# Optimization experiments

Hardware: AMD Instinct MI355X
Metric: run time of the kernel (lower is better)

The kernel has to match this reference:

```python
import jax, jax.numpy as jnp
import numpy as np

NUM_HEADS = 12
HEAD_DIM = 64
HIDDEN = NUM_HEADS * HEAD_DIM
AGENT_NUM = 40
MAX_POS = 2048
SCALE = HEAD_DIM ** -0.5


def _split_heads(x):
    # [b, s, hidden] -> [b, h, s, d]
    b, s, _ = x.shape
    return x.reshape(b, s, NUM_HEADS, HEAD_DIM).transpose(0, 2, 1, 3)


def _agent_pool(q, agent_num):
    # F.interpolate(q[None], size=(agent_num, dim), mode='bilinear', align_corners=False)
    # width (dim) is unchanged so it reduces to 1D linear interp along seq axis.
    b, s, dim = q.shape
    src = (jnp.arange(agent_num, dtype=q.dtype) + 0.5) * (s / agent_num) - 0.5
    src = jnp.clip(src, 0.0, s - 1.0)
    lo = jnp.floor(src).astype(jnp.int32)
    hi = jnp.minimum(lo + 1, s - 1)
    w = (src - lo.astype(q.dtype))[None, :, None]  # [1, A, 1]
    return q[:, lo, :] * (1.0 - w) + q[:, hi, :] * w  # [b, A, dim]


def setup_inputs() -> dict:
    key = jax.random.key(0)
    ks = jax.random.split(key, 6)
    bs, S = 16, 2048
    return {
        "hidden_states": jax.random.normal(ks[0], (bs, S, HIDDEN), jnp.float32),
        "attention_mask": jnp.zeros((bs, 1, 1, S), jnp.float32),
        "Wq": jax.random.normal(ks[1], (HIDDEN, HIDDEN), jnp.float32) * 0.02,
        "bq": jnp.zeros((HIDDEN,), jnp.float32),
        "Wk": jax.random.normal(ks[2], (HIDDEN, HIDDEN), jnp.float32) * 0.02,
        "bk": jnp.zeros((HIDDEN,), jnp.float32),
        "Wv": jax.random.normal(ks[3], (HIDDEN, HIDDEN), jnp.float32) * 0.02,
        "bv": jnp.zeros((HIDDEN,), jnp.float32),
        "dist_emb": jax.random.normal(ks[4], (2 * MAX_POS - 1, HEAD_DIM), jnp.float32) * 0.02,
    }


def reference(hidden_states, attention_mask, Wq, bq, Wk, bk, Wv, bv, dist_emb):
    bs, S, dim = hidden_states.shape
    q = hidden_states @ Wq + bq          # [b, S, hidden] (== query_layer flattened back)
    k = hidden_states @ Wk + bk
    v = hidden_states @ Wv + bv
    q_layer = _split_heads(q)            # [b, h, S, d]
    k_layer = _split_heads(k)
    v_layer = _split_heads(v)

    agent = _agent_pool(q, AGENT_NUM)    # [b, A, hidden]
    agent_layer = _split_heads(agent)    # [b, h, A, d]

    # stage 1: agent -> KV, with relative-key position bias
    d1 = jnp.arange(AGENT_NUM)[:, None] - jnp.arange(S)[None, :] + (MAX_POS - 1)
    pe1 = dist_emb[d1]                   # [A, S, d]
    bias1 = jnp.einsum('bhad,asd->bhas', agent_layer, pe1)
    score1 = jnp.einsum('bhad,bhsd->bhas', agent_layer * SCALE, k_layer) + bias1
    score1 = score1 + attention_mask     # [b,1,1,S] broadcasts over (h, A)
    p1 = jax.nn.softmax(score1, axis=-1)
    agent_v = jnp.einsum('bhas,bhsd->bhad', p1, v_layer)  # [b, h, A, d]

    # stage 2: query -> agents, with relative-key position bias
    d2 = jnp.arange(S)[:, None] - jnp.arange(AGENT_NUM)[None, :] + (MAX_POS - 1)
    pe2 = dist_emb[d2]                   # [S, A, d]
    bias2 = jnp.einsum('bhsd,sad->bhsa', q_layer, pe2)
    score2 = jnp.einsum('bhsd,bhad->bhsa', q_layer * SCALE, agent_layer) + bias2
    q_mask = jnp.swapaxes(attention_mask, -1, -2)  # [b,1,S,1]
    score2 = score2 + q_mask
    p2 = jax.nn.softmax(score2, axis=-1)
    x = jnp.einsum('bhsa,bhad->bhsd', p2, agent_v)  # [b, h, S, d]
    return x.transpose(0, 2, 1, 3).reshape(bs, S, dim)
```

## Files before the change

kernel.cpp:

```cpp
#include <hip/hip_runtime.h>
#include <math.h>

#define B_ 16
#define S_ 2048
#define H_ 12
#define D_ 64
#define HID 768
#define A_ 40
#define SCALE_ 0.125f
#define CH1 8
#define SUBT 64
#define NSUB 4

typedef __attribute__((ext_vector_type(8))) short short8v;
typedef __attribute__((ext_vector_type(4))) float f32x4;
typedef __attribute__((ext_vector_type(16))) float f32x16;

__device__ __forceinline__ unsigned f2bf_bits(float x) {
    unsigned u = __float_as_uint(x);
    return (u + 0x7FFFu + ((u >> 16) & 1u)) >> 16;
}

__device__ __forceinline__ void split1(float v, unsigned short& h, unsigned short& l) {
    __bf16 bh = (__bf16)v;
    float hf = (float)bh;
    __bf16 bl = (__bf16)(v - hf);
    h = __builtin_bit_cast(unsigned short, bh);
    l = __builtin_bit_cast(unsigned short, bl);
}

__device__ __forceinline__ void split8c(const float* x, int4& hi, int4& lo) {
    unsigned h[8], l[8];
#pragma unroll
    for (int i = 0; i < 8; i++) {
        __bf16 bh = (__bf16)x[i];
        float hf = (float)bh;
        __bf16 bl = (__bf16)(x[i] - hf);
        h[i] = (unsigned)__builtin_bit_cast(unsigned short, bh);
        l[i] = (unsigned)__builtin_bit_cast(unsigned short, bl);
    }
    hi = make_int4((int)(h[0] | (h[1] << 16)), (int)(h[2] | (h[3] << 16)),
                   (int)(h[4] | (h[5] << 16)), (int)(h[6] | (h[7] << 16)));
    lo = make_int4((int)(l[0] | (l[1] << 16)), (int)(l[2] | (l[3] << 16)),
                   (int)(l[4] | (l[5] << 16)), (int)(l[6] | (l[7] << 16)));
}

__global__ void wt_convert(const float* __restrict__ Wq, const float* __restrict__ Wk,
                           const float* __restrict__ Wv,
                           unsigned short* __restrict__ Wth, unsigned short* __restrict__ Wtl)
{
    int idx = blockIdx.x * 256 + threadIdx.x;
    if (idx >= 3 * 192 * 768) return;
    int n  = idx % 768;
    int kc = (idx / 768) % 192;
    int z  = idx / (768 * 192);
    const float* W = (z == 0) ? Wq : (z == 1) ? Wk : Wv;
    unsigned short h4[4], l4[4];
#pragma unroll
    for (int i = 0; i < 4; i++) {
        float x = W[(size_t)(4 * kc + i) * HID + n];
        unsigned hb = f2bf_bits(x);
        float hf = __uint_as_float(hb << 16);
        h4[i] = (unsigned short)hb;
        l4[i] = (unsigned short)f2bf_bits(x - hf);
    }
    size_t o = ((size_t)z * HID + n) * HID + 4 * kc;
    *(ushort4*)&Wth[o] = make_ushort4(h4[0], h4[1], h4[2], h4[3]);
    *(ushort4*)&Wtl[o] = make_ushort4(l4[0], l4[1], l4[2], l4[3]);
}

__global__ void dist_frag(const float* __restrict__ dist,
                          unsigned short* __restrict__ DFh, unsigned short* __restrict__ DFl)
{
    int g = blockIdx.x * 256 + threadIdx.x;
    if (g >= 256 * 2 * 64) return;
    int lane = g & 63;
    int ks = (g >> 6) & 1;
    int u  = g >> 7;
    int row = 8 + u * 16 + (lane & 15);
    int col = ks * 32 + ((lane >> 4) << 3);
    float xv[8];
#pragma unroll
    for (int j = 0; j < 8; j++)
        xv[j] = (row < 4095) ? dist[(size_t)row * D_ + col + j] : 0.f;
    int4 hi, lo;
    split8c(xv, hi, lo);
    *(int4*)&DFh[(size_t)g * 8] = hi;
    *(int4*)&DFl[(size_t)g * 8] = lo;
}

__global__ void dist_frag0(const float* __restrict__ dist,
                           unsigned short* __restrict__ Dh, unsigned short* __restrict__ Dl)
{
    int g = blockIdx.x * 256 + threadIdx.x;
    if (g >= 131 * 2 * 64) return;
    int lane = g & 63;
    int ks = (g >> 6) & 1;
    int u  = g >> 7;
    int row = u * 16 + (lane & 15);
    int col = ks * 32 + ((lane >> 4) << 3);
    float xv[8];
#pragma unroll
    for (int j = 0; j < 8; j++) xv[j] = dist[(size_t)row * D_ + col + j];
    int4 hi, lo;
    split8c(xv, hi, lo);
    *(int4*)&Dh[(size_t)g * 8] = hi;
    *(int4*)&Dl[(size_t)g * 8] = lo;
}

__global__ void ag_frag(const float* __restrict__ Ag,
                        unsigned short* __restrict__ Gh, unsigned short* __restrict__ Gl,
                        float scale)
{
    int g = blockIdx.x * 256 + threadIdx.x;
    if (g >= 192 * 3 * 2 * 64) return;
    int lane = g & 63;
    int r = g >> 6;
    int ks = r & 1; r >>= 1;
    int at = r % 3;
    int bh = r / 3;
    int a = at * 16 + (lane & 15);
    int col = ks * 32 + ((lane >> 4) << 3);
    float xv[8];
#pragma unroll
    for (int j = 0; j < 8; j++)
        xv[j] = (a < A_) ? scale * Ag[((size_t)bh * A_ + a) * D_ + col + j] : 0.f;
    int4 hi, lo;
    split8c(xv, hi, lo);
    *(int4*)&Gh[(size_t)g * 8] = hi;
    *(int4*)&Gl[(size_t)g * 8] = lo;
}

__global__ void avt_frag(const float* __restrict__ AgV,
                         unsigned short* __restrict__ Vh, unsigned short* __restrict__ Vl)
{
    int g = blockIdx.x * 256 + threadIdx.x;
    if (g >= 192 * 4 * 2 * 64) return;
    int lane = g & 63;
    int r = g >> 6;
    int ks = r & 1; r >>= 1;
    int nt = r & 3;
    int bh = r >> 2;
    int d = nt * 16 + (lane & 15);
    int a0 = ks * 32 + ((lane >> 4) << 3);
    float xv[8];
#pragma unroll
    for (int j = 0; j < 8; j++) {
        int a = a0 + j;
        xv[j] = (a < A_) ? AgV[((size_t)bh * A_ + a) * D_ + d] : 0.f;
    }
    int4 hi, lo;
    split8c(xv, hi, lo);
    *(int4*)&Vh[(size_t)g * 8] = hi;
    *(int4*)&Vl[(size_t)g * 8] = lo;
}

__global__ __launch_bounds__(512, 2) void qkv_z(
    const float* __restrict__ X,
    const unsigned short* __restrict__ Wth, const unsigned short* __restrict__ Wtl,
    const float* __restrict__ bq, const float* __restrict__ bk, const float* __restrict__ bv,
    float* __restrict__ Q, float* __restrict__ K, float* __restrict__ V)
{
    const int L   = blockIdx.x;
    const int k8  = L & 7, sl_ = L >> 3;
    const int mt  = k8 * 32 + sl_ / 9;
    const int sub = sl_ % 9;
    const int nt  = sub % 3, zz = sub / 3;
    const int m0 = mt * 128, n0 = nt * 256;

    const float* __restrict__ bias = (zz == 0) ? bq : (zz == 1) ? bk : bv;
    float* __restrict__ Out        = (zz == 0) ? Q  : (zz == 1) ? K  : V;
    const unsigned short* __restrict__ Bhg = Wth + (size_t)zz * HID * HID;
    const unsigned short* __restrict__ Blg = Wtl + (size_t)zz * HID * HID;

    __shared__ unsigned short Ah[128][40];
    __shared__ unsigned short Al[128][40];
    __shared__ unsigned short Bh[256][40];
    __shared__ unsigned short Bl[256][40];

    const int t = threadIdx.x;
    const int lane = t & 63, w = t >> 6;
    const int wm = (w & 1) * 64, wn = (w >> 1) * 64;
    const int r32 = lane & 31, kh = lane >> 5;

    const int sr = t >> 2, sca = (t & 3) * 8;
    const int sb = t >> 1, scb = (t & 1) * 16;

    f32x16 acc[2][2];
#pragma unroll
    for (int i = 0; i < 2; i++)
#pragma unroll
        for (int j = 0; j < 2; j++)
#pragma unroll
            for (int p = 0; p < 16; p++) acc[i][j][p] = 0.f;

    for (int k0 = 0; k0 < HID; k0 += 32) {
        float xv[8];
        const float* xp = X + (size_t)(m0 + sr) * HID + k0 + sca;
        float4 f0 = *(const float4*)xp;
        float4 f1 = *(const float4*)(xp + 4);
        xv[0] = f0.x; xv[1] = f0.y; xv[2] = f0.z; xv[3] = f0.w;
        xv[4] = f1.x; xv[5] = f1.y; xv[6] = f1.z; xv[7] = f1.w;
        int4 ah, al;
        split8c(xv, ah, al);
        size_t bo = (size_t)(n0 + sb) * HID + k0 + scb;
        int4 bh0 = *(const int4*)&Bhg[bo];
        int4 bh1 = *(const int4*)&Bhg[bo + 8];
        int4 bl0 = *(const int4*)&Blg[bo];
        int4 bl1 = *(const int4*)&Blg[bo + 8];

        __syncthreads();
        *(int4*)&Ah[sr][sca] = ah;
        *(int4*)&Al[sr][sca] = al;
        *(int4*)&Bh[sb][scb]     = bh0;  *(int4*)&Bh[sb][scb + 8] = bh1;
        *(int4*)&Bl[sb][scb]     = bl0;  *(int4*)&Bl[sb][scb + 8] = bl1;
        __syncthreads();

#pragma unroll
        for (int ks = 0; ks < 2; ks++) {
            const int ko = ks * 16 + kh * 8;
            short8v a_h[2], a_l[2], b_h[2], b_l[2];
#pragma unroll
            for (int i = 0; i < 2; i++) {
                a_h[i] = *(const short8v*)&Ah[wm + i * 32 + r32][ko];
                a_l[i] = *(const short8v*)&Al[wm + i * 32 + r32][ko];
                b_h[i] = *(const short8v*)&Bh[wn + i * 32 + r32][ko];
                b_l[i] = *(const short8v*)&Bl[wn + i * 32 + r32][ko];
            }
#pragma unroll
            for (int i = 0; i < 2; i++)
#pragma unroll
                for (int j = 0; j < 2; j++) {
                    acc[i][j] = __builtin_amdgcn_mfma_f32_32x32x16_bf16(a_h[i], b_h[j], acc[i][j], 0, 0, 0);
                    acc[i][j] = __builtin_amdgcn_mfma_f32_32x32x16_bf16(a_l[i], b_h[j], acc[i][j], 0, 0, 0);
                    acc[i][j] = __builtin_amdgcn_mfma_f32_32x32x16_bf16(a_h[i], b_l[j], acc[i][j], 0, 0, 0);
                }
        }
    }

    const float scl = (zz == 1) ? SCALE_ : 1.0f;
#pragma unroll
    for (int j = 0; j < 2; j++) {
        int n = n0 + wn + j * 32 + r32;
        float bj = bias[n];
        int h = n >> 6, d = n & 63;
#pragma unroll
        for (int i = 0; i < 2; i++) {
#pragma unroll
            for (int p = 0; p < 16; p++) {
                int m = m0 + wm + i * 32 + (p & 3) + 8 * (p >> 2) + 4 * kh;
                int b = m >> 11, s = m & 2047;
                Out[(((size_t)b * H_ + h) * S_ + s) * D_ + d] = (acc[i][j][p] + bj) * scl;
            }
        }
    }
}

__global__ void agent_pool(const float* __restrict__ Q, float* __restrict__ Ag)
{
    int idx = blockIdx.x * 256 + threadIdx.x;
    if (idx >= B_ * H_ * A_ * D_) return;
    int d  = idx & 63;
    int a  = (idx >> 6) % A_;
    int bh = idx / (A_ * D_);
    float src = ((float)a + 0.5f) * (2048.0f / 40.0f) - 0.5f;
    src = fminf(fmaxf(src, 0.0f), 2047.0f);
    int lo = (int)floorf(src);
    int hi = min(lo + 1, S_ - 1);
    float w = src - (float)lo;
    const float* base = Q + (size_t)bh * (S_ * D_);
    Ag[idx] = base[lo * D_ + d] * (1.0f - w) + base[hi * D_ + d] * w;
}

__global__ __launch_bounds__(256, 2) void stage1_mfma(
    const float* __restrict__ Kl, const float* __restrict__ Vl,
    const unsigned short* __restrict__ AG1h, const unsigned short* __restrict__ AG1l,
    const unsigned short* __restrict__ D0h,  const unsigned short* __restrict__ D0l,
    const float* __restrict__ mask,
    float* __restrict__ Pacc, float* __restrict__ Pm, float* __restrict__ Pl)
{
    const int q  = blockIdx.x;
    const int bh = blockIdx.y;
    const int b  = bh / H_;
    const int s0 = q * (NSUB * SUBT);
    const float* __restrict__ kb = Kl + (size_t)bh * (S_ * D_);
    const float* __restrict__ vb = Vl + (size_t)bh * (S_ * D_);

    __shared__ unsigned short KFh[4096], KFl[4096];
    __shared__ unsigned short VTh[4096], VTl[4096];
    __shared__ float sc[SUBT][52];
    __shared__ float scp[112][52];
    __shared__ float pm6[6][A_];
    __shared__ float mrow[A_], lrow[A_], resc[A_], mrw[SUBT];

    const int t = threadIdx.x;
    const int lane = t & 63, w = t >> 6;
    const int fr = lane & 15, kg = lane >> 4;

    if (t < A_) { mrow[t] = -INFINITY; lrow[t] = 0.0f; }

    f32x4 acc3[3];
#pragma unroll
    for (int at = 0; at < 3; at++) acc3[at] = (f32x4){0.f, 0.f, 0.f, 0.f};

    for (int st = 0; st < NSUB; st++) {
        const int sb = s0 + st * SUBT;
        const int u0 = (1984 - sb) >> 4;

        __syncthreads();

        {
            const int r = t >> 2, c0 = (t & 3) * 16;
            const float* kp = kb + (size_t)(sb + r) * D_ + c0;
            float xa[8], xb[8];
            float4 f0 = *(const float4*)(kp);
            float4 f1 = *(const float4*)(kp + 4);
            float4 f2 = *(const float4*)(kp + 8);
            float4 f3 = *(const float4*)(kp + 12);
            xa[0]=f0.x; xa[1]=f0.y; xa[2]=f0.z; xa[3]=f0.w;
            xa[4]=f1.x; xa[5]=f1.y; xa[6]=f1.z; xa[7]=f1.w;
            xb[0]=f2.x; xb[1]=f2.y; xb[2]=f2.z; xb[3]=f2.w;
            xb[4]=f3.x; xb[5]=f3.y; xb[6]=f3.z; xb[7]=f3.w;
            int4 h0, l0, h1, l1;
            split8c(xa, h0, l0);
            split8c(xb, h1, l1);
            const int tsr = r >> 4, frr = r & 15;
            const int c8a = (t & 3) * 2, c8b = c8a + 1;
            const int oa = ((tsr * 2 + (c8a >> 2)) * 64 + (((c8a & 3) << 4) | frr)) * 8;
            const int ob = ((tsr * 2 + (c8b >> 2)) * 64 + (((c8b & 3) << 4) | frr)) * 8;
            *(int4*)&KFh[oa] = h0;  *(int4*)&KFl[oa] = l0;
            *(int4*)&KFh[ob] = h1;  *(int4*)&KFl[ob] = l1;
        }
        {
            const int r = t >> 2, c0 = (t & 3) * 16;
            const float* vp = vb + (size_t)(sb + r) * D_ + c0;
            float vv[16];
            float4 g0 = *(const float4*)(vp);
            float4 g1 = *(const float4*)(vp + 4);
            float4 g2 = *(const float4*)(vp + 8);
            float4 g3 = *(const float4*)(vp + 12);
            vv[0]=g0.x; vv[1]=g0.y; vv[2]=g0.z; vv[3]=g0.w;
            vv[4]=g1.x; vv[5]=g1.y; vv[6]=g1.z; vv[7]=g1.w;
            vv[8]=g2.x; vv[9]=g2.y; vv[10]=g2.z; vv[11]=g2.w;
            vv[12]=g3.x; vv[13]=g3.y; vv[14]=g3.z; vv[15]=g3.w;
            const int ks2 = r >> 5, kgp = (r & 31) >> 3, e = r & 7;
#pragma unroll
            for (int jj = 0; jj < 16; jj++) {
                int d = c0 + jj;
                int off = (((d >> 4) * 2 + ks2) * 64 + kgp * 16 + (d & 15)) * 8 + e;
                unsigned short h, l;
                split1(vv[jj], h, l);
                VTh[off] = h; VTl[off] = l;
            }
        }
        if (t < SUBT) mrw[t] = mask[(size_t)b * S_ + sb + t];
        __syncthreads();

        {
            const int ts = w;
#pragma unroll
            for (int at = 0; at < 3; at++) {
                f32x4 a4 = (f32x4){0.f, 0.f, 0.f, 0.f};
#pragma unroll
                for (int ks = 0; ks < 2; ks++) {
                    size_t oA = ((((size_t)bh * 3 + at) * 2 + ks) * 64 + lane) * 8;
                    short8v gh = *(const short8v*)&AG1h[oA];
                    short8v gl = *(const short8v*)&AG1l[oA];
                    short8v kh2 = *(const short8v*)&KFh[((ts * 2 + ks) * 64 + lane) * 8];
                    short8v kl2 = *(const short8v*)&KFl[((ts * 2 + ks) * 64 + lane) * 8];
                    a4 = __builtin_amdgcn_mfma_f32_16x16x32_bf16(gh, kh2, a4, 0, 0, 0);
                    a4 = __builtin_amdgcn_mfma_f32_16x16x32_bf16(gl, kh2, a4, 0, 0, 0);
                    a4 = __builtin_amdgcn_mfma_f32_16x16x32_bf16(gh, kl2, a4, 0, 0, 0);
                }
                *(f32x4*)&sc[ts * 16 + fr][at * 16 + kg * 4] = a4;
            }
        }
        for (int ut = w; ut < 7; ut += 4) {
            const int u = u0 + ut;
#pragma unroll
            for (int at = 0; at < 3; at++) {
                f32x4 a4 = (f32x4){0.f, 0.f, 0.f, 0.f};
#pragma unroll
                for (int ks = 0; ks < 2; ks++) {
                    size_t oA = ((((size_t)bh * 3 + at) * 2 + ks) * 64 + lane) * 8;
                    short8v gh = *(const short8v*)&AG1h[oA];
                    short8v gl = *(const short8v*)&AG1l[oA];
                    size_t oD = (((size_t)u * 2 + ks) * 64 + lane) * 8;
                    short8v dh = *(const short8v*)&D0h[oD];
                    short8v dl = *(const short8v*)&D0l[oD];
                    a4 = __builtin_amdgcn_mfma_f32_16x16x32_bf16(gh, dh, a4, 0, 0, 0);
                    a4 = __builtin_amdgcn_mfma_f32_16x16x32_bf16(gl, dh, a4, 0, 0, 0);
                    a4 = __builtin_amdgcn_mfma_f32_16x16x32_bf16(gh, dl, a4, 0, 0, 0);
                }
                *(f32x4*)&scp[ut * 16 + fr][at * 16 + kg * 4] = a4;
            }
        }
        __syncthreads();

        for (int i = t; i < SUBT * A_; i += 256) {
            int rr = i / 40, aa = i - rr * 40;
            sc[rr][aa] += scp[aa + 63 - rr][aa] + mrw[rr];
        }
        __syncthreads();
        if (t < 240) {
            int a = t % 40, r6 = t / 40;
            float mx = -INFINITY;
            for (int i = r6; i < SUBT; i += 6) mx = fmaxf(mx, sc[i][a]);
            pm6[r6][a] = mx;
        }
        __syncthreads();
        if (t < A_) {
            float lm = pm6[0][t];
#pragma unroll
            for (int r6 = 1; r6 < 6; r6++) lm = fmaxf(lm, pm6[r6][t]);
            float mnew = fmaxf(mrow[t], lm);
            resc[t] = __expf(mrow[t] - mnew);
            mrow[t] = mnew;
        }
        __syncthreads();
        for (int i = t; i < SUBT * A_; i += 256) {
            int rr = i / 40, aa = i - rr * 40;
            sc[rr][aa] = __expf(sc[rr][aa] - mrow[aa]);
        }
        __syncthreads();
        if (t < 240) {
            int a = t % 40, r6 = t / 40;
            float sm = 0.0f;
            for (int i = r6; i < SUBT; i += 6) sm += sc[i][a];
            pm6[r6][a] = sm;
        }
        __syncthreads();
        if (t < A_) {
            float ls = pm6[0][t] + pm6[1][t] + pm6[2][t] + pm6[3][t] + pm6[4][t] + pm6[5][t];
            lrow[t] = lrow[t] * resc[t] + ls;
        }
        __syncthreads();

        for (int g = t; g < 384; g += 256) {
            int pl = g & 63;
            int c = g >> 6;
            int at = c >> 1, ks2 = c & 1;
            int a = at * 16 + (pl & 15);
            int sl0 = ks2 * 32 + (pl >> 4) * 8;
            float xv[8];
#pragma unroll
            for (int e = 0; e < 8; e++)
                xv[e] = (a < A_) ? sc[sl0 + e][a] : 0.f;
            int4 hi, lo;
            split8c(xv, hi, lo);
            *(int4*)&KFh[g * 8] = hi;
            *(int4*)&KFl[g * 8] = lo;
        }
        __syncthreads();

        {
            const int dt = w;
#pragma unroll
            for (int at = 0; at < 3; at++) {
                f32x4 a4 = acc3[at];
#pragma unroll
                for (int p = 0; p < 4; p++) {
                    int a = at * 16 + kg * 4 + p;
                    float rs = (a < A_) ? resc[a] : 0.f;
                    a4[p] *= rs;
                }
#pragma unroll
                for (int ks2 = 0; ks2 < 2; ks2++) {
                    short8v ph = *(const short8v*)&KFh[((at * 2 + ks2) * 64 + lane) * 8];
                    short8v pll = *(const short8v*)&KFl[((at * 2 + ks2) * 64 + lane) * 8];
                    short8v vh = *(const short8v*)&VTh[((dt * 2 + ks2) * 64 + lane) * 8];
                    short8v vl = *(const short8v*)&VTl[((dt * 2 + ks2) * 64 + lane) * 8];
                    a4 = __builtin_amdgcn_mfma_f32_16x16x32_bf16(ph, vh, a4, 0, 0, 0);
                    a4 = __builtin_amdgcn_mfma_f32_16x16x32_bf16(pll, vh, a4, 0, 0, 0);
                    a4 = __builtin_amdgcn_mfma_f32_16x16x32_bf16(ph, vl, a4, 0, 0, 0);
                }
                acc3[at] = a4;
            }
        }
    }
    __syncthreads();

    {
        const int dt = w;
#pragma unroll
        for (int at = 0; at < 3; at++) {
#pragma unroll
            for (int p = 0; p < 4; p++) {
                int a = at * 16 + kg * 4 + p;
                if (a < A_)
                    Pacc[(((size_t)(bh * CH1 + q) * A_) + a) * D_ + dt * 16 + fr] = acc3[at][p];
            }
        }
    }
    if (t < A_) {
        Pm[(size_t)(bh * CH1 + q) * A_ + t] = mrow[t];
        Pl[(size_t)(bh * CH1 + q) * A_ + t] = lrow[t];
    }
}

__global__ __launch_bounds__(256) void stage1_reduce(
    const float* __restrict__ Pacc, const float* __restrict__ Pm,
    const float* __restrict__ Pl, float* __restrict__ AgV)
{
    const int bh = blockIdx.x;
    const int t = threadIdx.x;
    __shared__ float F[CH1][A_], Linv[A_];
    if (t < A_) {
        float M = -INFINITY;
#pragma unroll
        for (int q = 0; q < CH1; q++) M = fmaxf(M, Pm[(size_t)(bh * CH1 + q) * A_ + t]);
        float L = 0.0f;
#pragma unroll
        for (int q = 0; q < CH1; q++) {
            float f = __expf(Pm[(size_t)(bh * CH1 + q) * A_ + t] - M);
            F[q][t] = f;
            L = fmaf(f, Pl[(size_t)(bh * CH1 + q) * A_ + t], L);
        }
        Linv[t] = 1.0f / L;
    }
    __syncthreads();
#pragma unroll
    for (int ii = 0; ii < 3; ii++) {
        int i = t + ii * 256;
        if (i < A_ * 16) {
            int a = i >> 4, d4 = i & 15;
            float4 s4 = make_float4(0.f, 0.f, 0.f, 0.f);
            for (int q = 0; q < CH1; q++) {
                float f = F[q][a];
                float4 p4 = *(const float4*)&Pacc[(((size_t)(bh * CH1 + q) * A_) + a) * D_ + d4 * 4];
                s4.x = fmaf(f, p4.x, s4.x);
                s4.y = fmaf(f, p4.y, s4.y);
                s4.z = fmaf(f, p4.z, s4.z);
                s4.w = fmaf(f, p4.w, s4.w);
            }
            float inv = Linv[a];
            s4.x *= inv; s4.y *= inv; s4.z *= inv; s4.w *= inv;
            *(float4*)&AgV[(size_t)bh * (A_ * D_) + a * D_ + d4 * 4] = s4;
        }
    }
}

__global__ __launch_bounds__(256, 2) void stage2_mfma(
    const float* __restrict__ Qg,
    const unsigned short* __restrict__ AGFh, const unsigned short* __restrict__ AGFl,
    const unsigned short* __restrict__ DFh,  const unsigned short* __restrict__ DFl,
    const unsigned short* __restrict__ AVFh, const unsigned short* __restrict__ AVFl,
    float* __restrict__ Out)
{
    const int sbk = blockIdx.x;
    const int bh  = blockIdx.y;
    const int b = bh / H_, h = bh % H_;
    const int s0 = sbk * 64;
    const int base_u = 4 * sbk + 125;

    __shared__ unsigned short Qfh[8 * 64 * 8], Qfl[8 * 64 * 8];
    __shared__ float scm[64][52];
    __shared__ float scp[64][68];
    __shared__ unsigned short PAh[64][72], PAl[64][72];

    const int t = threadIdx.x;
    const int lane = t & 63, ts = t >> 6;
    const int fr = lane & 15, kg = lane >> 4;

    {
        const int r = t >> 2, c0 = (t & 3) * 16;
        const float* qp = Qg + ((size_t)bh * S_ + s0 + r) * D_ + c0;
        float xa[8], xb[8];
        float4 f0 = *(const float4*)(qp);
        float4 f1 = *(const float4*)(qp + 4);
        float4 f2 = *(const float4*)(qp + 8);
        float4 f3 = *(const float4*)(qp + 12);
        xa[0]=f0.x; xa[1]=f0.y; xa[2]=f0.z; xa[3]=f0.w;
        xa[4]=f1.x; xa[5]=f1.y; xa[6]=f1.z; xa[7]=f1.w;
        xb[0]=f2.x; xb[1]=f2.y; xb[2]=f2.z; xb[3]=f2.w;
        xb[4]=f3.x; xb[5]=f3.y; xb[6]=f3.z; xb[7]=f3.w;
        int4 h0, l0, h1, l1;
        split8c(xa, h0, l0);
        split8c(xb, h1, l1);
        const int tsr = r >> 4, frr = r & 15;
        const int c8a = (t & 3) * 2, c8b = c8a + 1;
        const int oa = ((tsr * 2 + (c8a >> 2)) * 64 + (((c8a & 3) << 4) | frr)) * 8;
        const int ob = ((tsr * 2 + (c8b >> 2)) * 64 + (((c8b & 3) << 4) | frr)) * 8;
        *(int4*)&Qfh[oa] = h0;  *(int4*)&Qfl[oa] = l0;
        *(int4*)&Qfh[ob] = h1;  *(int4*)&Qfl[ob] = l1;
    }
    __syncthreads();

    short8v qh[2], ql[2];
#pragma unroll
    for (int ks = 0; ks < 2; ks++) {
        qh[ks] = *(const short8v*)&Qfh[((ts * 2 + ks) * 64 + lane) * 8];
        ql[ks] = *(const short8v*)&Qfl[((ts * 2 + ks) * 64 + lane) * 8];
    }

#pragma unroll
    for (int at = 0; at < 3; at++) {
        f32x4 acc = (f32x4){0.f, 0.f, 0.f, 0.f};
#pragma unroll
        for (int ks = 0; ks < 2; ks++) {
            size_t o = ((((size_t)bh * 3 + at) * 2 + ks) * 64 + lane) * 8;
            short8v chv = *(const short8v*)&AGFh[o];
            short8v clv = *(const short8v*)&AGFl[o];
            acc = __builtin_amdgcn_mfma_f32_16x16x32_bf16(chv, qh[ks], acc, 0, 0, 0);
            acc = __builtin_amdgcn_mfma_f32_16x16x32_bf16(clv, qh[ks], acc, 0, 0, 0);
            acc = __builtin_amdgcn_mfma_f32_16x16x32_bf16(chv, ql[ks], acc, 0, 0, 0);
        }
        *(f32x4*)&scm[ts * 16 + fr][at * 16 + kg * 4] = acc;
    }
#pragma unroll
    for (int o4 = 0; o4 < 4; o4++) {
        f32x4 acc = (f32x4){0.f, 0.f, 0.f, 0.f};
        const int u = base_u + ts + o4;
#pragma unroll
        for (int ks = 0; ks < 2; ks++) {
            size_t o = (((size_t)u * 2 + ks) * 64 + lane) * 8;
            short8v chv = *(const short8v*)&DFh[o];
            short8v clv = *(const short8v*)&DFl[o];
            acc = __builtin_amdgcn_mfma_f32_16x16x32_bf16(chv, qh[ks], acc, 0, 0, 0);
            acc = __builtin_amdgcn_mfma_f32_16x16x32_bf16(clv, qh[ks], acc, 0, 0, 0);
            acc = __builtin_amdgcn_mfma_f32_16x16x32_bf16(chv, ql[ks], acc, 0, 0, 0);
        }
        *(f32x4*)&scp[ts * 16 + fr][o4 * 16 + kg * 4] = acc;
    }
    __syncthreads();

    {
        const int r = t >> 2, dq = t & 3;
        const int base = (r & 15) + 39;
        float val[10];
#pragma unroll
        for (int i = 0; i < 10; i++) {
            int a = dq * 10 + i;
            val[i] = scm[r][a] + scp[r][base - a];
        }
        float mx = -INFINITY;
#pragma unroll
        for (int i = 0; i < 10; i++) mx = fmaxf(mx, val[i]);
        mx = fmaxf(mx, __shfl_xor(mx, 1));
        mx = fmaxf(mx, __shfl_xor(mx, 2));
        float sum = 0.f;
#pragma unroll
        for (int i = 0; i < 10; i++) { val[i] = __expf(val[i] - mx); sum += val[i]; }
        sum += __shfl_xor(sum, 1);
        sum += __shfl_xor(sum, 2);
        float inv = 1.0f / sum;
        unsigned* ph = (unsigned*)&PAh[r][0];
        unsigned* pl = (unsigned*)&PAl[r][0];
#pragma unroll
        for (int i = 0; i < 5; i++) {
            unsigned short h0, l0, h1, l1;
            split1(val[2 * i] * inv, h0, l0);
            split1(val[2 * i + 1] * inv, h1, l1);
            ph[dq * 5 + i] = (unsigned)h0 | ((unsigned)h1 << 16);
            pl[dq * 5 + i] = (unsigned)l0 | ((unsigned)l1 << 16);
        }
#pragma unroll
        for (int i = 0; i < 3; i++) { ph[20 + dq * 3 + i] = 0u; pl[20 + dq * 3 + i] = 0u; }
    }
    __syncthreads();

    short8v ph8[2], pl8[2];
#pragma unroll
    for (int ks = 0; ks < 2; ks++) {
        ph8[ks] = *(const short8v*)&PAh[ts * 16 + fr][ks * 32 + kg * 8];
        pl8[ks] = *(const short8v*)&PAl[ts * 16 + fr][ks * 32 + kg * 8];
    }
#pragma unroll
    for (int nt = 0; nt < 4; nt++) {
        f32x4 acc = (f32x4){0.f, 0.f, 0.f, 0.f};
#pragma unroll
        for (int ks = 0; ks < 2; ks++) {
            size_t o = ((((size_t)bh * 4 + nt) * 2 + ks) * 64 + lane) * 8;
            short8v vh = *(const short8v*)&AVFh[o];
            short8v vl = *(const short8v*)&AVFl[o];
            acc = __builtin_amdgcn_mfma_f32_16x16x32_bf16(ph8[ks], vh, acc, 0, 0, 0);
            acc = __builtin_amdgcn_mfma_f32_16x16x32_bf16(pl8[ks], vh, acc, 0, 0, 0);
            acc = __builtin_amdgcn_mfma_f32_16x16x32_bf16(ph8[ks], vl, acc, 0, 0, 0);
        }
        const int d = nt * 16 + fr;
        float* op = Out + ((size_t)b * S_ + s0 + ts * 16 + kg * 4) * HID + h * D_ + d;
#pragma unroll
        for (int r = 0; r < 4; r++)
            op[(size_t)r * HID] = acc[r];
    }
}

extern "C" void kernel_launch(void* const* d_in, const int* in_sizes, int n_in,
                              void* d_out, int out_size, void* d_ws, size_t ws_size,
                              hipStream_t stream) {
    const float* hs   = (const float*)d_in[0];
    const float* mask = (const float*)d_in[1];
    const float* Wq   = (const float*)d_in[2];
    const float* bq   = (const float*)d_in[3];
    const float* Wk   = (const float*)d_in[4];
    const float* bk   = (const float*)d_in[5];
    const float* Wv   = (const float*)d_in[6];
    const float* bv   = (const float*)d_in[7];
    const float* dist = (const float*)d_in[8];
    float* out = (float*)d_out;

    float* ws = (float*)d_ws;
    const size_t QKV = (size_t)B_ * H_ * S_ * D_;
    const size_t AG  = (size_t)B_ * H_ * A_ * D_;
    float* Q     = ws;
    float* K     = ws + QKV;
    float* V     = ws + 2 * QKV;
    float* Agent = ws + 3 * QKV;
    float* AgV   = Agent + AG;
    float* Pacc  = AgV + AG;
    float* Pm    = Pacc + (size_t)B_ * H_ * CH1 * A_ * D_;
    float* Pl    = Pm + (size_t)B_ * H_ * CH1 * A_;
    unsigned short* Wth = (unsigned short*)(Pl + (size_t)B_ * H_ * CH1 * A_);
    unsigned short* Wtl = Wth + (size_t)3 * HID * HID;
    unsigned short* DFh = Wtl + (size_t)3 * HID * HID;
    unsigned short* DFl = DFh + (size_t)262144;
    unsigned short* AGFh = DFl + (size_t)262144;
    unsigned short* AGFl = AGFh + (size_t)589824;
    unsigned short* AVFh = AGFl + (size_t)589824;
    unsigned short* AVFl = AVFh + (size_t)786432;
    unsigned short* AG1h = AVFl + (size_t)786432;
    unsigned short* AG1l = AG1h + (size_t)589824;
    unsigned short* D0h  = AG1l + (size_t)589824;
    unsigned short* D0l  = D0h + (size_t)134144;

    wt_convert<<<(3 * 192 * 768 + 255) / 256, 256, 0, stream>>>(Wq, Wk, Wv, Wth, Wtl);
    dist_frag<<<(256 * 2 * 64 + 255) / 256, 256, 0, stream>>>(dist, DFh, DFl);
    dist_frag0<<<(131 * 2 * 64 + 255) / 256, 256, 0, stream>>>(dist, D0h, D0l);
    qkv_z<<<2304, 512, 0, stream>>>(hs, Wth, Wtl, bq, bk, bv, Q, K, V);
    agent_pool<<<(B_ * H_ * A_ * D_ + 255) / 256, 256, 0, stream>>>(Q, Agent);
    ag_frag<<<(192 * 3 * 2 * 64 + 255) / 256, 256, 0, stream>>>(Agent, AGFh, AGFl, SCALE_);
    ag_frag<<<(192 * 3 * 2 * 64 + 255) / 256, 256, 0, stream>>>(Agent, AG1h, AG1l, 1.0f);
    dim3 g1(CH1, B_ * H_);
    stage1_mfma<<<g1, 256, 0, stream>>>(K, V, AG1h, AG1l, D0h, D0l, mask, Pacc, Pm, Pl);
    stage1_reduce<<<B_ * H_, 256, 0, stream>>>(Pacc, Pm, Pl, AgV);
    avt_frag<<<(192 * 4 * 2 * 64 + 255) / 256, 256, 0, stream>>>(AgV, AVFh, AVFl);
    dim3 g2(32, B_ * H_);
    stage2_mfma<<<g2, 256, 0, stream>>>(Q, AGFh, AGFl, DFh, DFl, AVFh, AVFl, out);
}
```

Baseline: 578.5 us.

## Process four query chunks per stage2 block with register-cached agents and Q prefetch

Each stage2 block now handles 256 sequence positions in four 64-row chunks instead of one, so the grid shrinks from 32 to 8 blocks per (batch, head). The agent fragments are loaded into registers once per block and reused across chunks. The next chunk's Q rows are prefetched from global memory during the current chunk's MFMA work. This cuts redundant agent loads and launch overhead, at the cost of fewer blocks (1536 total), more register pressure, and extra barriers per chunk.

```diff
diff --git a/kernel.cpp b/kernel.cpp
--- a/kernel.cpp
+++ b/kernel.cpp
@@ -547,11 +547,9 @@
     const unsigned short* __restrict__ AVFh, const unsigned short* __restrict__ AVFl,
     float* __restrict__ Out)
 {
-    const int sbk = blockIdx.x;
+    const int sb8 = blockIdx.x;
     const int bh  = blockIdx.y;
     const int b = bh / H_, h = bh % H_;
-    const int s0 = sbk * 64;
-    const int base_u = 4 * sbk + 125;
 
     __shared__ unsigned short Qfh[8 * 64 * 8], Qfl[8 * 64 * 8];
     __shared__ float scm[64][52];
@@ -562,126 +560,154 @@
     const int lane = t & 63, ts = t >> 6;
     const int fr = lane & 15, kg = lane >> 4;
 
+    short8v agh[3][2], agl[3][2];
+#pragma unroll
+    for (int at = 0; at < 3; at++)
+#pragma unroll
+        for (int ks = 0; ks < 2; ks++) {
+            size_t o = ((((size_t)bh * 3 + at) * 2 + ks) * 64 + lane) * 8;
+            agh[at][ks] = *(const short8v*)&AGFh[o];
+            agl[at][ks] = *(const short8v*)&AGFl[o];
+        }
+
+    const int r = t >> 2, c0 = (t & 3) * 16;
+    const int tsr = r >> 4, frr = r & 15;
+    const int c8a = (t & 3) * 2, c8b = c8a + 1;
+    const int oa = ((tsr * 2 + (c8a >> 2)) * 64 + (((c8a & 3) << 4) | frr)) * 8;
+    const int ob = ((tsr * 2 + (c8b >> 2)) * 64 + (((c8b & 3) << 4) | frr)) * 8;
+    const float* qbase = Qg + ((size_t)bh * S_ + sb8 * 256 + r) * D_ + c0;
+
     {
-        const int r = t >> 2, c0 = (t & 3) * 16;
-        const float* qp = Qg + ((size_t)bh * S_ + s0 + r) * D_ + c0;
-        float xa[8], xb[8];
-        float4 f0 = *(const float4*)(qp);
-        float4 f1 = *(const float4*)(qp + 4);
-        float4 f2 = *(const float4*)(qp + 8);
-        float4 f3 = *(const float4*)(qp + 12);
-        xa[0]=f0.x; xa[1]=f0.y; xa[2]=f0.z; xa[3]=f0.w;
-        xa[4]=f1.x; xa[5]=f1.y; xa[6]=f1.z; xa[7]=f1.w;
-        xb[0]=f2.x; xb[1]=f2.y; xb[2]=f2.z; xb[3]=f2.w;
-        xb[4]=f3.x; xb[5]=f3.y; xb[6]=f3.z; xb[7]=f3.w;
+        float4 f0 = *(const float4*)(qbase);
+        float4 f1 = *(const float4*)(qbase + 4);
+        float4 f2 = *(const float4*)(qbase + 8);
+        float4 f3 = *(const float4*)(qbase + 12);
+        float xa[8] = {f0.x, f0.y, f0.z, f0.w, f1.x, f1.y, f1.z, f1.w};
+        float xb[8] = {f2.x, f2.y, f2.z, f2.w, f3.x, f3.y, f3.z, f3.w};
         int4 h0, l0, h1, l1;
         split8c(xa, h0, l0);
         split8c(xb, h1, l1);
-        const int tsr = r >> 4, frr = r & 15;
-        const int c8a = (t & 3) * 2, c8b = c8a + 1;
-        const int oa = ((tsr * 2 + (c8a >> 2)) * 64 + (((c8a & 3) << 4) | frr)) * 8;
-        const int ob = ((tsr * 2 + (c8b >> 2)) * 64 + (((c8b & 3) << 4) | frr)) * 8;
         *(int4*)&Qfh[oa] = h0;  *(int4*)&Qfl[oa] = l0;
         *(int4*)&Qfh[ob] = h1;  *(int4*)&Qfl[ob] = l1;
     }
     __syncthreads();
 
-    short8v qh[2], ql[2];
-#pragma unroll
-    for (int ks = 0; ks < 2; ks++) {
-        qh[ks] = *(const short8v*)&Qfh[((ts * 2 + ks) * 64 + lane) * 8];
-        ql[ks] = *(const short8v*)&Qfl[((ts * 2 + ks) * 64 + lane) * 8];
-    }
-
-#pragma unroll
-    for (int at = 0; at < 3; at++) {
-        f32x4 acc = (f32x4){0.f, 0.f, 0.f, 0.f};
+    for (int c = 0; c < 4; c++) {
+        const int s0 = sb8 * 256 + c * 64;
+        const int base_u = (s0 >> 4) + 125;
+
+        short8v qh[2], ql[2];
 #pragma unroll
         for (int ks = 0; ks < 2; ks++) {
-            size_t o = ((((size_t)bh * 3 + at) * 2 + ks) * 64 + lane) * 8;
-            short8v chv = *(const short8v*)&AGFh[o];
-            short8v clv = *(const short8v*)&AGFl[o];
-            acc = __builtin_amdgcn_mfma_f32_16x16x32_bf16(chv, qh[ks], acc, 0, 0, 0);
-            acc = __builtin_amdgcn_mfma_f32_16x16x32_bf16(clv, qh[ks], acc, 0, 0, 0);
-            acc = __builtin_amdgcn_mfma_f32_16x16x32_bf16(chv, ql[ks], acc, 0, 0, 0);
-        }
-        *(f32x4*)&scm[ts * 16 + fr][at * 16 + kg * 4] = acc;
-    }
-#pragma unroll
-    for (int o4 = 0; o4 < 4; o4++) {
-        f32x4 acc = (f32x4){0.f, 0.f, 0.f, 0.f};
-        const int u = base_u + ts + o4;
+            qh[ks] = *(const short8v*)&Qfh[((ts * 2 + ks) * 64 + lane) * 8];
+            ql[ks] = *(const short8v*)&Qfl[((ts * 2 + ks) * 64 + lane) * 8];
+        }
+        float4 nf0, nf1, nf2, nf3;
+        if (c < 3) {
+            const float* np = qbase + (size_t)(c + 1) * 64 * D_;
+            nf0 = *(const float4*)(np);
+            nf1 = *(const float4*)(np + 4);
+            nf2 = *(const float4*)(np + 8);
+            nf3 = *(const float4*)(np + 12);
+        }
+
+#pragma unroll
+        for (int at = 0; at < 3; at++) {
+            f32x4 acc = (f32x4){0.f, 0.f, 0.f, 0.f};
+#pragma unroll
+            for (int ks = 0; ks < 2; ks++) {
+                acc = __builtin_amdgcn_mfma_f32_16x16x32_bf16(agh[at][ks], qh[ks], acc, 0, 0, 0);
+                acc = __builtin_amdgcn_mfma_f32_16x16x32_bf16(agl[at][ks], qh[ks], acc, 0, 0, 0);
+                acc = __builtin_amdgcn_mfma_f32_16x16x32_bf16(agh[at][ks], ql[ks], acc, 0, 0, 0);
+            }
+            *(f32x4*)&scm[ts * 16 + fr][at * 16 + kg * 4] = acc;
+        }
+#pragma unroll
+        for (int o4 = 0; o4 < 4; o4++) {
+            f32x4 acc = (f32x4){0.f, 0.f, 0.f, 0.f};
+            const int u = base_u + ts + o4;
+#pragma unroll
+            for (int ks = 0; ks < 2; ks++) {
+                size_t o = (((size_t)u * 2 + ks) * 64 + lane) * 8;
+                short8v chv = *(const short8v*)&DFh[o];
+                short8v clv = *(const short8v*)&DFl[o];
+                acc = __builtin_amdgcn_mfma_f32_16x16x32_bf16(chv, qh[ks], acc, 0, 0, 0);
+                acc = __builtin_amdgcn_mfma_f32_16x16x32_bf16(clv, qh[ks], acc, 0, 0, 0);
+                acc = __builtin_amdgcn_mfma_f32_16x16x32_bf16(chv, ql[ks], acc, 0, 0, 0);
+            }
+            *(f32x4*)&scp[ts * 16 + fr][o4 * 16 + kg * 4] = acc;
+        }
+        __syncthreads();
+
+        if (c < 3) {
+            float xa[8] = {nf0.x, nf0.y, nf0.z, nf0.w, nf1.x, nf1.y, nf1.z, nf1.w};
+            float xb[8] = {nf2.x, nf2.y, nf2.z, nf2.w, nf3.x, nf3.y, nf3.z, nf3.w};
+            int4 h0, l0, h1, l1;
+            split8c(xa, h0, l0);
+            split8c(xb, h1, l1);
+            *(int4*)&Qfh[oa] = h0;  *(int4*)&Qfl[oa] = l0;
+            *(int4*)&Qfh[ob] = h1;  *(int4*)&Qfl[ob] = l1;
+        }
+        {
+            const int rr = t >> 2, dq = t & 3;
+            const int base = (rr & 15) + 39;
+            float val[10];
+#pragma unroll
+            for (int i = 0; i < 10; i++) {
+                int a = dq * 10 + i;
+                val[i] = scm[rr][a] + scp[rr][base - a];
+            }
+            float mx = -INFINITY;
+#pragma unroll
+            for (int i = 0; i < 10; i++) mx = fmaxf(mx, val[i]);
+            mx = fmaxf(mx, __shfl_xor(mx, 1));
+            mx = fmaxf(mx, __shfl_xor(mx, 2));
+            float sum = 0.f;
+#pragma unroll
+            for (int i = 0; i < 10; i++) { val[i] = __expf(val[i] - mx); sum += val[i]; }
+            sum += __shfl_xor(sum, 1);
+            sum += __shfl_xor(sum, 2);
+            float inv = 1.0f / sum;
+            unsigned* ph = (unsigned*)&PAh[rr][0];
+            unsigned* pl = (unsigned*)&PAl[rr][0];
+#pragma unroll
+            for (int i = 0; i < 5; i++) {
+                unsigned short h0, l0, h1, l1;
+                split1(val[2 * i] * inv, h0, l0);
+                split1(val[2 * i + 1] * inv, h1, l1);
+                ph[dq * 5 + i] = (unsigned)h0 | ((unsigned)h1 << 16);
+                pl[dq * 5 + i] = (unsigned)l0 | ((unsigned)l1 << 16);
+            }
+#pragma unroll
+            for (int i = 0; i < 3; i++) { ph[20 + dq * 3 + i] = 0u; pl[20 + dq * 3 + i] = 0u; }
+        }
+        __syncthreads();
+
+        short8v ph8[2], pl8[2];
 #pragma unroll
         for (int ks = 0; ks < 2; ks++) {
-            size_t o = (((size_t)u * 2 + ks) * 64 + lane) * 8;
-            short8v chv = *(const short8v*)&DFh[o];
-            short8v clv = *(const short8v*)&DFl[o];
-            acc = __builtin_amdgcn_mfma_f32_16x16x32_bf16(chv, qh[ks], acc, 0, 0, 0);
-            acc = __builtin_amdgcn_mfma_f32_16x16x32_bf16(clv, qh[ks], acc, 0, 0, 0);
-            acc = __builtin_amdgcn_mfma_f32_16x16x32_bf16(chv, ql[ks], acc, 0, 0, 0);
-        }
-        *(f32x4*)&scp[ts * 16 + fr][o4 * 16 + kg * 4] = acc;
-    }
-    __syncthreads();
-
-    {
-        const int r = t >> 2, dq = t & 3;
-        const int base = (r & 15) + 39;
-        float val[10];
-#pragma unroll
-        for (int i = 0; i < 10; i++) {
-            int a = dq * 10 + i;
-            val[i] = scm[r][a] + scp[r][base - a];
-        }
-        float mx = -INFINITY;
-#pragma unroll
-        for (int i = 0; i < 10; i++) mx = fmaxf(mx, val[i]);
-        mx = fmaxf(mx, __shfl_xor(mx, 1));
-        mx = fmaxf(mx, __shfl_xor(mx, 2));
-        float sum = 0.f;
-#pragma unroll
-        for (int i = 0; i < 10; i++) { val[i] = __expf(val[i] - mx); sum += val[i]; }
-        sum += __shfl_xor(sum, 1);
-        sum += __shfl_xor(sum, 2);
-        float inv = 1.0f / sum;
-        unsigned* ph = (unsigned*)&PAh[r][0];
-        unsigned* pl = (unsigned*)&PAl[r][0];
-#pragma unroll
-        for (int i = 0; i < 5; i++) {
-            unsigned short h0, l0, h1, l1;
-            split1(val[2 * i] * inv, h0, l0);
-            split1(val[2 * i + 1] * inv, h1, l1);
-            ph[dq * 5 + i] = (unsigned)h0 | ((unsigned)h1 << 16);
-            pl[dq * 5 + i] = (unsigned)l0 | ((unsigned)l1 << 16);
-        }
-#pragma unroll
-        for (int i = 0; i < 3; i++) { ph[20 + dq * 3 + i] = 0u; pl[20 + dq * 3 + i] = 0u; }
-    }
-    __syncthreads();
-
-    short8v ph8[2], pl8[2];
-#pragma unroll
-    for (int ks = 0; ks < 2; ks++) {
-        ph8[ks] = *(const short8v*)&PAh[ts * 16 + fr][ks * 32 + kg * 8];
-        pl8[ks] = *(const short8v*)&PAl[ts * 16 + fr][ks * 32 + kg * 8];
-    }
-#pragma unroll
-    for (int nt = 0; nt < 4; nt++) {
-        f32x4 acc = (f32x4){0.f, 0.f, 0.f, 0.f};
-#pragma unroll
-        for (int ks = 0; ks < 2; ks++) {
-            size_t o = ((((size_t)bh * 4 + nt) * 2 + ks) * 64 + lane) * 8;
-            short8v vh = *(const short8v*)&AVFh[o];
-            short8v vl = *(const short8v*)&AVFl[o];
-            acc = __builtin_amdgcn_mfma_f32_16x16x32_bf16(ph8[ks], vh, acc, 0, 0, 0);
-            acc = __builtin_amdgcn_mfma_f32_16x16x32_bf16(pl8[ks], vh, acc, 0, 0, 0);
-            acc = __builtin_amdgcn_mfma_f32_16x16x32_bf16(ph8[ks], vl, acc, 0, 0, 0);
-        }
-        const int d = nt * 16 + fr;
-        float* op = Out + ((size_t)b * S_ + s0 + ts * 16 + kg * 4) * HID + h * D_ + d;
-#pragma unroll
-        for (int r = 0; r < 4; r++)
-            op[(size_t)r * HID] = acc[r];
+            ph8[ks] = *(const short8v*)&PAh[ts * 16 + fr][ks * 32 + kg * 8];
+            pl8[ks] = *(const short8v*)&PAl[ts * 16 + fr][ks * 32 + kg * 8];
+        }
+#pragma unroll
+        for (int nt = 0; nt < 4; nt++) {
+            f32x4 acc = (f32x4){0.f, 0.f, 0.f, 0.f};
+#pragma unroll
+            for (int ks = 0; ks < 2; ks++) {
+                size_t o = ((((size_t)bh * 4 + nt) * 2 + ks) * 64 + lane) * 8;
+                short8v vh = *(const short8v*)&AVFh[o];
+                short8v vl = *(const short8v*)&AVFl[o];
+                acc = __builtin_amdgcn_mfma_f32_16x16x32_bf16(ph8[ks], vh, acc, 0, 0, 0);
+                acc = __builtin_amdgcn_mfma_f32_16x16x32_bf16(pl8[ks], vh, acc, 0, 0, 0);
+                acc = __builtin_amdgcn_mfma_f32_16x16x32_bf16(ph8[ks], vl, acc, 0, 0, 0);
+            }
+            const int d = nt * 16 + fr;
+            float* op = Out + ((size_t)b * S_ + s0 + ts * 16 + kg * 4) * HID + h * D_ + d;
+#pragma unroll
+            for (int rr = 0; rr < 4; rr++)
+                op[(size_t)rr * HID] = acc[rr];
+        }
+        __syncthreads();
     }
 }
 
@@ -734,6 +760,6 @@
     stage1_mfma<<<g1, 256, 0, stream>>>(K, V, AG1h, AG1l, D0h, D0l, mask, Pacc, Pm, Pl);
     stage1_reduce<<<B_ * H_, 256, 0, stream>>>(Pacc, Pm, Pl, AgV);
     avt_frag<<<(192 * 4 * 2 * 64 + 255) / 256, 256, 0, stream>>>(AgV, AVFh, AVFl);
-    dim3 g2(32, B_ * H_);
+    dim3 g2(8, B_ * H_);
     stage2_mfma<<<g2, 256, 0, stream>>>(Q, AGFh, AGFl, DFh, DFl, AVFh, AVFl, out);
 }
```

Measured after the change: 563.4 us. 1.03x faster.
